# Optimization experiments

Measured on AMD Instinct MI355X. Metric: run time of the kernel, lower is better.

The kernel has to match this reference:

```python
import jax, jax.numpy as jnp
import numpy as np

B, T, C = 4, 2048, 1024
H = 16
D = C // H  # head_dim = 64


def setup_inputs() -> dict:
    key = jax.random.key(0)
    k1, k2, k3 = jax.random.split(key, 3)
    x = jax.random.normal(k1, (B, T, C), dtype=jnp.float32)
    w_qkv = jax.random.normal(k2, (C, 3 * C), dtype=jnp.float32) * (C ** -0.5)
    b_qkv = jnp.zeros((3 * C,), dtype=jnp.float32)
    w_proj = jax.random.normal(k3, (C, C), dtype=jnp.float32) * (C ** -0.5)
    b_proj = jnp.zeros((C,), dtype=jnp.float32)
    return {"x": x, "w_qkv": w_qkv, "b_qkv": b_qkv, "w_proj": w_proj, "b_proj": b_proj}


def reference(x, w_qkv, b_qkv, w_proj, b_proj):
    # qkv projection: (B,T,C) -> (B,T,3,H,D) -> q,k,v each (B,H,T,D)
    qkv = (x @ w_qkv + b_qkv).reshape(B, T, 3, H, D)
    q, k, v = jnp.moveaxis(qkv, 2, 0)           # each (B, T, H, D)
    q = q.transpose(0, 2, 1, 3)                 # (B, H, T, D)
    k = k.transpose(0, 2, 1, 3)
    v = v.transpose(0, 2, 1, 3)

    scale = 1.0 / jnp.sqrt(jnp.float32(D))
    attn = jnp.einsum('bhqd,bhkd->bhqk', q, k) * scale  # (B,H,T,T)
    causal = jnp.tril(jnp.ones((T, T), dtype=bool))
    attn = jnp.where(causal[None, None], attn, -jnp.inf)
    attn = jax.nn.softmax(attn, axis=-1)
    # dropout p=0.0 (eval mode) -> identity
    out = jnp.einsum('bhqk,bhkd->bhqd', attn, v)        # (B,H,T,D)
    out = out.transpose(0, 2, 1, 3).reshape(B, T, C)
    return out @ w_proj + b_proj
```

## Files before the change

kernel.cpp:

```cpp
#include <hip/hip_runtime.h>
#include <hip/hip_bf16.h>


#define Bsz 4
#define Tsz 2048
#define Csz 1024
#define Hn  16
#define Dh  64

typedef unsigned short u16;
typedef __attribute__((ext_vector_type(8))) short bf16x8;
typedef __attribute__((ext_vector_type(4))) float f32x4;
typedef __attribute__((ext_vector_type(4))) unsigned int u32x4;
typedef __attribute__((ext_vector_type(2))) unsigned int u32x2;

__device__ __forceinline__ u16 f2b(float f) {
  __hip_bfloat16 h = __float2bfloat16(f);
  return *reinterpret_cast<u16*>(&h);
}

__device__ __forceinline__ void gld_lds16(const void* g, void* lds) {
  __builtin_amdgcn_global_load_lds(
      (const __attribute__((address_space(1))) unsigned int*)g,
      (__attribute__((address_space(3))) unsigned int*)lds, 16, 0, 0);
}

__global__ __launch_bounds__(256) void cvt_f32_bf16(const float* __restrict__ in,
                                                    u16* __restrict__ out) {
  size_t i = ((size_t)blockIdx.x * 256 + threadIdx.x) * 8;
  f32x4 a = *(const f32x4*)(in + i);
  f32x4 b = *(const f32x4*)(in + i + 4);
  u16 r[8];
#pragma unroll
  for (int j = 0; j < 4; ++j) { r[j] = f2b(a[j]); r[4 + j] = f2b(b[j]); }
  *(u32x4*)(out + i) = *(const u32x4*)r;
}

__global__ __launch_bounds__(256) void cvt_transpose(const float* __restrict__ in,
                                                     u16* __restrict__ out,
                                                     int R, int C) {
  __shared__ u16 tile[64 * 66];
  const int r0 = blockIdx.x * 64, c0 = blockIdx.y * 64;
  const int tid = threadIdx.x;
#pragma unroll
  for (int i = 0; i < 16; ++i) {
    int idx = i * 256 + tid;
    int r = idx >> 6, c = idx & 63;
    tile[r * 66 + c] = f2b(in[(size_t)(r0 + r) * C + (c0 + c)]);
  }
  __syncthreads();
#pragma unroll
  for (int i = 0; i < 16; ++i) {
    int idx = i * 256 + tid;
    int c = idx >> 6, r = idx & 63;
    out[(size_t)(c0 + c) * R + (r0 + r)] = tile[r * 66 + c];
  }
}

__device__ __forceinline__ void gemm_tile_acc(const u16* __restrict__ A,
                                              const u16* __restrict__ Bt,
                                              int m0, int n0,
                                              u16* Alds, u16* Blds,
                                              f32x4 acc[4][4]) {
  const int tid = threadIdx.x;
  const int w = tid >> 6, lane = tid & 63;
  const int wm = w & 1, wn = w >> 1;
  const int col = lane & 15, quad = lane >> 4;
  const int lrow = lane >> 2;
  const int kseg = (lane & 3) * 8;
#pragma unroll
  for (int mt = 0; mt < 4; ++mt)
#pragma unroll
    for (int nt = 0; nt < 4; ++nt)
      acc[mt][nt] = (f32x4){0.f, 0.f, 0.f, 0.f};

  for (int k0 = 0; k0 < 1024; k0 += 32) {
    __syncthreads();
#pragma unroll
    for (int g = 0; g < 2; ++g) {
      int grp = w * 2 + g;
      gld_lds16(A + (size_t)(m0 + grp * 16 + lrow) * 1024 + k0 + kseg,
                (char*)Alds + grp * 1024);
      gld_lds16(Bt + (size_t)(n0 + grp * 16 + lrow) * 1024 + k0 + kseg,
                (char*)Blds + grp * 1024);
    }
    __syncthreads();
    bf16x8 af[4], bfr[4];
#pragma unroll
    for (int mt = 0; mt < 4; ++mt)
      af[mt] = *(const bf16x8*)(Alds + (wm * 64 + mt * 16 + col) * 32 + quad * 8);
#pragma unroll
    for (int nt = 0; nt < 4; ++nt)
      bfr[nt] = *(const bf16x8*)(Blds + (wn * 64 + nt * 16 + col) * 32 + quad * 8);
#pragma unroll
    for (int mt = 0; mt < 4; ++mt)
#pragma unroll
      for (int nt = 0; nt < 4; ++nt)
        acc[mt][nt] = __builtin_amdgcn_mfma_f32_16x16x32_bf16(af[mt], bfr[nt],
                                                              acc[mt][nt], 0, 0, 0);
  }
}

__global__ __launch_bounds__(256) void gemm_qkv(const u16* __restrict__ X,
                                                const u16* __restrict__ WT,
                                                const float* __restrict__ bias,
                                                u16* __restrict__ Q,
                                                u16* __restrict__ Kc,
                                                u16* __restrict__ Vt) {
  __shared__ __align__(16) u16 Alds[128 * 32];
  __shared__ __align__(16) u16 Blds[128 * 32];
  f32x4 acc[4][4];
  const int m0 = blockIdx.x * 128, n0 = blockIdx.y * 128;
  gemm_tile_acc(X, WT, m0, n0, Alds, Blds, acc);

  const float qscale = 0.18033688011112042f;
  const int tid = threadIdx.x;
  const int w = tid >> 6, lane = tid & 63;
  const int wm = w & 1, wn = w >> 1;
  const int col = lane & 15, quad = lane >> 4;
#pragma unroll
  for (int mt = 0; mt < 4; ++mt)
#pragma unroll
    for (int nt = 0; nt < 4; ++nt) {
      int n = n0 + wn * 64 + nt * 16 + col;
      int s = n >> 10, hh = (n >> 6) & (Hn - 1), d = n & 63;
      int mBase = m0 + wm * 64 + mt * 16 + quad * 4;
      int b = mBase >> 11, t0 = mBase & (Tsz - 1);
      if (s == 2) {
        u16 vals[4];
#pragma unroll
        for (int r = 0; r < 4; ++r) vals[r] = f2b(acc[mt][nt][r] + bias[n]);
        *(u32x2*)(Vt + ((size_t)(b * Hn + hh) * Dh + d) * Tsz + t0) =
            *(const u32x2*)vals;
      } else {
        const float scl = (s == 0) ? qscale : 1.f;
        u16* dst = (s == 0) ? Q : Kc;
#pragma unroll
        for (int r = 0; r < 4; ++r)
          dst[((size_t)(b * Hn + hh) * Tsz + (t0 + r)) * Dh + d] =
              f2b((acc[mt][nt][r] + bias[n]) * scl);
      }
    }
}

__global__ __launch_bounds__(256) void gemm_proj(const u16* __restrict__ O,
                                                 const u16* __restrict__ WT,
                                                 const float* __restrict__ bias,
                                                 float* __restrict__ out) {
  __shared__ __align__(16) u16 Alds[128 * 32];
  __shared__ __align__(16) u16 Blds[128 * 32];
  f32x4 acc[4][4];
  const int m0 = blockIdx.x * 128, n0 = blockIdx.y * 128;
  gemm_tile_acc(O, WT, m0, n0, Alds, Blds, acc);

  const int tid = threadIdx.x;
  const int w = tid >> 6, lane = tid & 63;
  const int wm = w & 1, wn = w >> 1;
  const int col = lane & 15, quad = lane >> 4;
#pragma unroll
  for (int mt = 0; mt < 4; ++mt)
#pragma unroll
    for (int nt = 0; nt < 4; ++nt)
#pragma unroll
      for (int r = 0; r < 4; ++r) {
        int m = m0 + wm * 64 + mt * 16 + quad * 4 + r;
        int n = n0 + wn * 64 + nt * 16 + col;
        out[(size_t)m * Csz + n] = acc[mt][nt][r] + bias[n];
      }
}

#define PSTR 40
__global__ __launch_bounds__(256, 8) void attn(const u16* __restrict__ Q,
                                               const u16* __restrict__ Kg,
                                               const u16* __restrict__ Vt,
                                               u16* __restrict__ O) {
  __shared__ __align__(16) u16 Ps[64 * PSTR];
  __shared__ __align__(16) u16 Ks[2][32 * 64];
  __shared__ __align__(16) u16 Vs[2][64 * 32];

  const int d0 = blockIdx.x + (blockIdx.y << 5) + (blockIdx.z << 9);
  const int xcd = d0 & 7, rest = d0 >> 3;
  const int j = rest & 31, ghi = rest >> 5;
  const int bh = (ghi << 3) + xcd;
  const int qt = 31 - j;
  const int h = bh & (Hn - 1), b = bh >> 4;

  const int tid = threadIdx.x, w = tid >> 6, lane = tid & 63;
  const int col = lane & 15, quad = lane >> 4;
  const int qbase = qt * 64;

  const u16* Kbase = Kg + (size_t)bh * Tsz * Dh;
  const u16* Vbase = Vt + (size_t)bh * Dh * Tsz;

  const u16* Qg = Q + ((size_t)bh * Tsz + qbase) * Dh;
  bf16x8 aq[2];
#pragma unroll
  for (int ks = 0; ks < 2; ++ks)
    aq[ks] = *(const bf16x8*)(Qg + (size_t)(w * 16 + col) * Dh + ks * 32 + quad * 8);

  const int kswz = (tid >> 3) * 64 + (((tid & 7) ^ ((tid >> 3) & 7)) << 3);
  const int vd = tid >> 2, vseg = (tid & 3) * 8;

  f32x4 oacc[4];
#pragma unroll
  for (int dt = 0; dt < 4; ++dt) oacc[dt] = (f32x4){0.f, 0.f, 0.f, 0.f};
  float lsum[4] = {0.f, 0.f, 0.f, 0.f};

  const int nst = 2 * qt + 2;
  const int sdiag = 2 * qt;

  gld_lds16(Kbase + kswz, &Ks[0][w * 512]);
  gld_lds16(Vbase + (size_t)vd * Tsz + vseg, &Vs[0][w * 512]);

  for (int s = 0; s < nst; ++s) {
    __syncthreads();
    const int cur = s & 1;
    if (s + 1 < nst) {
      const int nxt = cur ^ 1;
      gld_lds16(Kbase + (size_t)(s + 1) * 2048 + kswz, &Ks[nxt][w * 512]);
      gld_lds16(Vbase + (size_t)vd * Tsz + (s + 1) * 32 + vseg, &Vs[nxt][w * 512]);
    }

    f32x4 sacc[2];
#pragma unroll
    for (int nt = 0; nt < 2; ++nt) sacc[nt] = (f32x4){0.f, 0.f, 0.f, 0.f};
#pragma unroll
    for (int ks = 0; ks < 2; ++ks)
#pragma unroll
      for (int nt = 0; nt < 2; ++nt) {
        bf16x8 bk = *(const bf16x8*)(
            &Ks[cur][(nt * 16 + col) * 64 + ((((ks * 4 + quad) ^ (col & 7))) << 3)]);
        sacc[nt] = __builtin_amdgcn_mfma_f32_16x16x32_bf16(aq[ks], bk,
                                                           sacc[nt], 0, 0, 0);
      }

    if (s >= sdiag) {
#pragma unroll
      for (int nt = 0; nt < 2; ++nt)
#pragma unroll
        for (int r = 0; r < 4; ++r) {
          int rl = w * 16 + quad * 4 + r;
          int cg = s * 32 + nt * 16 + col;
          float p = (cg > qbase + rl) ? 0.f : exp2f(sacc[nt][r]);
          lsum[r] += p;
          Ps[rl * PSTR + nt * 16 + col] = f2b(p);
        }
    } else {
#pragma unroll
      for (int nt = 0; nt < 2; ++nt)
#pragma unroll
        for (int r = 0; r < 4; ++r) {
          int rl = w * 16 + quad * 4 + r;
          float p = exp2f(sacc[nt][r]);
          lsum[r] += p;
          Ps[rl * PSTR + nt * 16 + col] = f2b(p);
        }
    }
    __threadfence_block();

    bf16x8 ap = *(const bf16x8*)(&Ps[(w * 16 + col) * PSTR + quad * 8]);
#pragma unroll
    for (int dt = 0; dt < 4; ++dt) {
      bf16x8 bv = *(const bf16x8*)(&Vs[cur][(dt * 16 + col) * 32 + quad * 8]);
      oacc[dt] = __builtin_amdgcn_mfma_f32_16x16x32_bf16(ap, bv,
                                                         oacc[dt], 0, 0, 0);
    }
  }

#pragma unroll
  for (int r = 0; r < 4; ++r) {
    float v = lsum[r];
#pragma unroll
    for (int off = 1; off < 16; off <<= 1) v += __shfl_xor(v, off);
    lsum[r] = v;
  }

#pragma unroll
  for (int r = 0; r < 4; ++r) {
    float inv = 1.0f / lsum[r];
    int rg = qbase + w * 16 + quad * 4 + r;
#pragma unroll
    for (int dt = 0; dt < 4; ++dt) {
      int d = dt * 16 + col;
      O[(((size_t)b * Tsz + rg) * Hn + h) * Dh + d] = f2b(oacc[dt][r] * inv);
    }
  }
}

extern "C" void kernel_launch(void* const* d_in, const int* in_sizes, int n_in,
                              void* d_out, int out_size, void* d_ws, size_t ws_size,
                              hipStream_t stream) {
  const float* x      = (const float*)d_in[0];
  const float* w_qkv  = (const float*)d_in[1];
  const float* b_qkv  = (const float*)d_in[2];
  const float* w_proj = (const float*)d_in[3];
  const float* b_proj = (const float*)d_in[4];
  float* out = (float*)d_out;

  u16* Xb     = (u16*)d_ws;
  u16* WqkvT  = Xb + (size_t)8192 * 1024;
  u16* WprojT = WqkvT + (size_t)3072 * 1024;
  u16* Qb     = WprojT + (size_t)1024 * 1024;
  u16* Kb     = Qb + (size_t)8192 * 1024;
  u16* Ob     = Kb + (size_t)8192 * 1024;
  u16* Vtb    = (u16*)d_out;

  cvt_f32_bf16<<<4096, 256, 0, stream>>>(x, Xb);
  cvt_transpose<<<dim3(16, 48), 256, 0, stream>>>(w_qkv, WqkvT, 1024, 3072);
  cvt_transpose<<<dim3(16, 16), 256, 0, stream>>>(w_proj, WprojT, 1024, 1024);
  gemm_qkv<<<dim3(64, 24), 256, 0, stream>>>(Xb, WqkvT, b_qkv, Qb, Kb, Vtb);
  attn<<<dim3(32, 16, 4), 256, 0, stream>>>(Qb, Kb, Vtb, Ob);
  gemm_proj<<<dim3(64, 8), 256, 0, stream>>>(Ob, WprojT, b_proj, out);
}
```

Baseline: 286.3 us.

## Keep attention probabilities in registers via permlane swaps, widen key tiles to 64

The attention kernel no longer stages the softmax probabilities through a shared-memory P buffer. It computes S transposed (K as the A operand) so each lane holds a query column, then packs the probabilities to bf16 and rearranges them in registers with permlane32/permlane16 swaps into the A-operand layout for the PV MFMA. Key/value tiles grow from 32 to 64 keys per step, with a swizzled V layout and half as many loop iterations and barriers. Occupancy hint drops from 8 to 5 blocks to allow the larger LDS and register footprint, and output stores become 8-byte vector writes.

```diff
diff --git a/kernel.cpp b/kernel.cpp
--- a/kernel.cpp
+++ b/kernel.cpp
@@ -17,6 +17,10 @@
 __device__ __forceinline__ u16 f2b(float f) {
   __hip_bfloat16 h = __float2bfloat16(f);
   return *reinterpret_cast<u16*>(&h);
+}
+
+__device__ __forceinline__ unsigned pk2(float lo, float hi) {
+  return (unsigned)f2b(lo) | ((unsigned)f2b(hi) << 16);
 }
 
 __device__ __forceinline__ void gld_lds16(const void* g, void* lds) {
@@ -169,14 +173,12 @@
       }
 }
 
-#define PSTR 40
-__global__ __launch_bounds__(256, 8) void attn(const u16* __restrict__ Q,
+__global__ __launch_bounds__(256, 5) void attn(const u16* __restrict__ Q,
                                                const u16* __restrict__ Kg,
                                                const u16* __restrict__ Vt,
                                                u16* __restrict__ O) {
-  __shared__ __align__(16) u16 Ps[64 * PSTR];
-  __shared__ __align__(16) u16 Ks[2][32 * 64];
-  __shared__ __align__(16) u16 Vs[2][64 * 32];
+  __shared__ __align__(16) u16 Ks[2][64 * 64];
+  __shared__ __align__(16) u16 Vs[2][64 * 64];
 
   const int d0 = blockIdx.x + (blockIdx.y << 5) + (blockIdx.z << 9);
   const int xcd = d0 & 7, rest = d0 >> 3;
@@ -198,92 +200,106 @@
   for (int ks = 0; ks < 2; ++ks)
     aq[ks] = *(const bf16x8*)(Qg + (size_t)(w * 16 + col) * Dh + ks * 32 + quad * 8);
 
-  const int kswz = (tid >> 3) * 64 + (((tid & 7) ^ ((tid >> 3) & 7)) << 3);
-  const int vd = tid >> 2, vseg = (tid & 3) * 8;
+  const int xseg = ((tid & 7) ^ ((tid >> 3) & 7)) * 8;
+  const size_t koff = (size_t)(tid >> 3) * 64 + xseg;
+  const size_t voff = (size_t)(tid >> 3) * Tsz + xseg;
+  const int swz = col & 7;
 
   f32x4 oacc[4];
 #pragma unroll
   for (int dt = 0; dt < 4; ++dt) oacc[dt] = (f32x4){0.f, 0.f, 0.f, 0.f};
-  float lsum[4] = {0.f, 0.f, 0.f, 0.f};
-
-  const int nst = 2 * qt + 2;
-  const int sdiag = 2 * qt;
-
-  gld_lds16(Kbase + kswz, &Ks[0][w * 512]);
-  gld_lds16(Vbase + (size_t)vd * Tsz + vseg, &Vs[0][w * 512]);
+  float lsum = 0.f;
+
+  const int nst = qt + 1;
+  gld_lds16(Kbase + koff, &Ks[0][w * 512]);
+  gld_lds16(Kbase + 2048 + koff, &Ks[0][2048 + w * 512]);
+  gld_lds16(Vbase + voff, &Vs[0][w * 512]);
+  gld_lds16(Vbase + (size_t)32 * Tsz + voff, &Vs[0][2048 + w * 512]);
 
   for (int s = 0; s < nst; ++s) {
     __syncthreads();
     const int cur = s & 1;
     if (s + 1 < nst) {
       const int nxt = cur ^ 1;
-      gld_lds16(Kbase + (size_t)(s + 1) * 2048 + kswz, &Ks[nxt][w * 512]);
-      gld_lds16(Vbase + (size_t)vd * Tsz + (s + 1) * 32 + vseg, &Vs[nxt][w * 512]);
-    }
-
-    f32x4 sacc[2];
-#pragma unroll
-    for (int nt = 0; nt < 2; ++nt) sacc[nt] = (f32x4){0.f, 0.f, 0.f, 0.f};
+      gld_lds16(Kbase + (size_t)(s + 1) * 4096 + koff, &Ks[nxt][w * 512]);
+      gld_lds16(Kbase + (size_t)(s + 1) * 4096 + 2048 + koff,
+                &Ks[nxt][2048 + w * 512]);
+      gld_lds16(Vbase + (size_t)(s + 1) * 64 + voff, &Vs[nxt][w * 512]);
+      gld_lds16(Vbase + (size_t)(s + 1) * 64 + (size_t)32 * Tsz + voff,
+                &Vs[nxt][2048 + w * 512]);
+    }
+
+    f32x4 sacc[4];
+#pragma unroll
+    for (int kt = 0; kt < 4; ++kt) sacc[kt] = (f32x4){0.f, 0.f, 0.f, 0.f};
 #pragma unroll
     for (int ks = 0; ks < 2; ++ks)
 #pragma unroll
-      for (int nt = 0; nt < 2; ++nt) {
+      for (int kt = 0; kt < 4; ++kt) {
         bf16x8 bk = *(const bf16x8*)(
-            &Ks[cur][(nt * 16 + col) * 64 + ((((ks * 4 + quad) ^ (col & 7))) << 3)]);
-        sacc[nt] = __builtin_amdgcn_mfma_f32_16x16x32_bf16(aq[ks], bk,
-                                                           sacc[nt], 0, 0, 0);
+            &Ks[cur][(kt * 16 + col) * 64 + (((ks * 4 + quad) ^ swz) << 3)]);
+        sacc[kt] = __builtin_amdgcn_mfma_f32_16x16x32_bf16(bk, aq[ks],
+                                                           sacc[kt], 0, 0, 0);
       }
 
-    if (s >= sdiag) {
-#pragma unroll
-      for (int nt = 0; nt < 2; ++nt)
+    float e[4][4];
+    if (s == qt) {
+      const int qg = w * 16 + col;
+#pragma unroll
+      for (int kt = 0; kt < 4; ++kt)
 #pragma unroll
         for (int r = 0; r < 4; ++r) {
-          int rl = w * 16 + quad * 4 + r;
-          int cg = s * 32 + nt * 16 + col;
-          float p = (cg > qbase + rl) ? 0.f : exp2f(sacc[nt][r]);
-          lsum[r] += p;
-          Ps[rl * PSTR + nt * 16 + col] = f2b(p);
+          int kl = kt * 16 + quad * 4 + r;
+          float p = (kl > qg) ? 0.f : exp2f(sacc[kt][r]);
+          lsum += p;
+          e[kt][r] = p;
         }
     } else {
 #pragma unroll
-      for (int nt = 0; nt < 2; ++nt)
+      for (int kt = 0; kt < 4; ++kt)
 #pragma unroll
         for (int r = 0; r < 4; ++r) {
-          int rl = w * 16 + quad * 4 + r;
-          float p = exp2f(sacc[nt][r]);
-          lsum[r] += p;
-          Ps[rl * PSTR + nt * 16 + col] = f2b(p);
+          float p = exp2f(sacc[kt][r]);
+          lsum += p;
+          e[kt][r] = p;
         }
     }
-    __threadfence_block();
-
-    bf16x8 ap = *(const bf16x8*)(&Ps[(w * 16 + col) * PSTR + quad * 8]);
-#pragma unroll
-    for (int dt = 0; dt < 4; ++dt) {
-      bf16x8 bv = *(const bf16x8*)(&Vs[cur][(dt * 16 + col) * 32 + quad * 8]);
-      oacc[dt] = __builtin_amdgcn_mfma_f32_16x16x32_bf16(ap, bv,
-                                                         oacc[dt], 0, 0, 0);
-    }
-  }
-
-#pragma unroll
-  for (int r = 0; r < 4; ++r) {
-    float v = lsum[r];
-#pragma unroll
-    for (int off = 1; off < 16; off <<= 1) v += __shfl_xor(v, off);
-    lsum[r] = v;
-  }
-
-#pragma unroll
-  for (int r = 0; r < 4; ++r) {
-    float inv = 1.0f / lsum[r];
-    int rg = qbase + w * 16 + quad * 4 + r;
-#pragma unroll
-    for (int dt = 0; dt < 4; ++dt) {
-      int d = dt * 16 + col;
-      O[(((size_t)b * Tsz + rg) * Hn + h) * Dh + d] = f2b(oacc[dt][r] * inv);
-    }
+
+#pragma unroll
+    for (int ksg = 0; ksg < 2; ++ksg) {
+      unsigned w00 = pk2(e[2 * ksg][0], e[2 * ksg][1]);
+      unsigned w01 = pk2(e[2 * ksg][2], e[2 * ksg][3]);
+      unsigned w10 = pk2(e[2 * ksg + 1][0], e[2 * ksg + 1][1]);
+      unsigned w11 = pk2(e[2 * ksg + 1][2], e[2 * ksg + 1][3]);
+      auto ra = __builtin_amdgcn_permlane32_swap(w00, w10, false, false);
+      auto rb = __builtin_amdgcn_permlane32_swap(w01, w11, false, false);
+      auto sa = __builtin_amdgcn_permlane16_swap(ra[0], ra[1], false, false);
+      auto sb = __builtin_amdgcn_permlane16_swap(rb[0], rb[1], false, false);
+      union { unsigned u[4]; bf16x8 v; } pf;
+      pf.u[0] = sa[0]; pf.u[1] = sb[0]; pf.u[2] = sa[1]; pf.u[3] = sb[1];
+#pragma unroll
+      for (int dt = 0; dt < 4; ++dt) {
+        bf16x8 bv = *(const bf16x8*)(
+            &Vs[cur][(dt * 16 + col) * 64 + (((ksg * 4 + quad) ^ swz) << 3)]);
+        oacc[dt] = __builtin_amdgcn_mfma_f32_16x16x32_bf16(bv, pf.v,
+                                                           oacc[dt], 0, 0, 0);
+      }
+    }
+  }
+
+  float v = lsum;
+  v += __shfl_xor(v, 16);
+  v += __shfl_xor(v, 32);
+  const float inv = 1.0f / v;
+
+  const int rg = qbase + w * 16 + col;
+  u16* Orow = O + (((size_t)b * Tsz + rg) * Hn + h) * Dh;
+#pragma unroll
+  for (int dt = 0; dt < 4; ++dt) {
+    u16 vals[4];
+#pragma unroll
+    for (int r = 0; r < 4; ++r) vals[r] = f2b(oacc[dt][r] * inv);
+    *(u32x2*)(Orow + dt * 16 + quad * 4) = *(const u32x2*)vals;
   }
 }
 
```

After: 288.8 us. No clear change (+0.9%).
